# Performance work log

Hardware: AMD Instinct MI355X
Metric: run time of the kernel (lower is better)

Reference implementation:

```python
import jax, jax.numpy as jnp
import numpy as np

B, S, D = 8, 1024, 1152
H = 16
HD = D // H
HID = int(D * 4.0)
LN_EPS = 1e-5


def layer_norm(x, w, b):
    m = jnp.mean(x, axis=-1, keepdims=True)
    v = jnp.mean(jnp.square(x - m), axis=-1, keepdims=True)
    return (x - m) * jax.lax.rsqrt(v + LN_EPS) * w + b


def modulate(x, shift, scale):
    # shift/scale: [B, D] broadcast over seq
    return x * (1.0 + scale[:, None, :]) + shift[:, None, :]


def setup_inputs() -> dict:
    key = jax.random.key(0)
    ks = jax.random.split(key, 16)
    s = 0.02
    return {
        "x": jax.random.normal(ks[0], (B, S, D), jnp.float32),
        "c": jax.random.normal(ks[1], (B, D), jnp.float32),
        "ln1_w": jnp.ones((D,), jnp.float32),
        "ln1_b": jnp.zeros((D,), jnp.float32),
        "wq": jax.random.normal(ks[2], (D, D), jnp.float32) * s,
        "wk": jax.random.normal(ks[3], (D, D), jnp.float32) * s,
        "wv": jax.random.normal(ks[4], (D, D), jnp.float32) * s,
        "wo": jax.random.normal(ks[5], (D, D), jnp.float32) * s,
        "wo_b": jnp.zeros((D,), jnp.float32),
        "ln2_w": jnp.ones((D,), jnp.float32),
        "ln2_b": jnp.zeros((D,), jnp.float32),
        "fc1_w": jax.random.normal(ks[6], (D, HID), jnp.float32) * s,
        "fc1_b": jnp.zeros((HID,), jnp.float32),
        "fc2_w": jax.random.normal(ks[7], (HID, D), jnp.float32) * s,
        "fc2_b": jnp.zeros((D,), jnp.float32),
        "ada_w": jax.random.normal(ks[8], (D, 6 * D), jnp.float32) * s,
        "ada_b": jnp.zeros((6 * D,), jnp.float32),
    }


def attention(x, wq, wk, wv, wo, wo_b):
    b, s, d = x.shape
    q = (x @ wq).reshape(b, s, H, HD).transpose(0, 2, 1, 3)  # [B,H,S,hd]
    k = (x @ wk).reshape(b, s, H, HD).transpose(0, 2, 1, 3)
    v = (x @ wv).reshape(b, s, H, HD).transpose(0, 2, 1, 3)
    scale = 1.0 / np.sqrt(HD).astype(np.float32)
    att = jnp.einsum("bhqd,bhkd->bhqk", q, k) * scale
    att = jax.nn.softmax(att, axis=-1)
    out = jnp.einsum("bhqk,bhkd->bhqd", att, v)
    out = out.transpose(0, 2, 1, 3).reshape(b, s, d)
    return out @ wo + wo_b


def reference(x, c, ln1_w, ln1_b, wq, wk, wv, wo, wo_b, ln2_w, ln2_b,
              fc1_w, fc1_b, fc2_w, fc2_b, ada_w, ada_b):
    mod = jax.nn.silu(c) @ ada_w + ada_b  # [B, 6D]
    sh_msa, sc_msa, g_msa, sh_mlp, sc_mlp, g_mlp = jnp.split(mod, 6, axis=1)
    h = modulate(layer_norm(x, ln1_w, ln1_b), sh_msa, sc_msa)
    x = x + g_msa[:, None, :] * attention(h, wq, wk, wv, wo, wo_b)
    h = modulate(layer_norm(x, ln2_w, ln2_b), sh_mlp, sc_mlp)
    h = jax.nn.gelu(h @ fc1_w + fc1_b, approximate=False) @ fc2_w + fc2_b
    x = x + g_mlp[:, None, :] * h
    return x
```

## Files before the change

kernel.cpp:

```cpp
#include <hip/hip_runtime.h>
#include <hip/hip_bf16.h>


typedef unsigned short u16;
typedef unsigned int u32;
typedef __attribute__((ext_vector_type(8))) short bf16x8;
typedef __attribute__((ext_vector_type(4))) float f32x4;

#define MFMA16(a, b, c) __builtin_amdgcn_mfma_f32_16x16x32_bf16((a), (b), (c), 0, 0, 0)

__device__ __forceinline__ u16 f2bf(float f) {
  __hip_bfloat16 h = __float2bfloat16(f);
  return __builtin_bit_cast(u16, h);
}

__device__ __forceinline__ void gload16(const u16* g, u16* l) {
  __builtin_amdgcn_global_load_lds(
      (const __attribute__((address_space(1))) unsigned int*)(const void*)g,
      (__attribute__((address_space(3))) unsigned int*)(void*)l, 16, 0, 0);
}

__global__ void k_silu(const float* __restrict__ c, float* __restrict__ o, int n) {
  int i = blockIdx.x * 256 + threadIdx.x;
  if (i < n) { float v = c[i]; o[i] = v / (1.f + __expf(-v)); }
}

__global__ __launch_bounds__(256) void k_modproj1(const float* __restrict__ sc,
                                                  const float* __restrict__ aw,
                                                  float* __restrict__ partial) {
  __shared__ float lc[8][144];
  int kc = blockIdx.y;
  for (int i = threadIdx.x; i < 1152; i += 256) {
    int b = i / 144, k = i % 144;
    lc[b][k] = sc[b * 1152 + kc * 144 + k];
  }
  __syncthreads();
  int j = blockIdx.x * 256 + threadIdx.x;
  float acc[8] = {0, 0, 0, 0, 0, 0, 0, 0};
  for (int k = 0; k < 144; ++k) {
    float w = aw[(size_t)(kc * 144 + k) * 6912 + j];
    #pragma unroll
    for (int b = 0; b < 8; ++b) acc[b] += lc[b][k] * w;
  }
  #pragma unroll
  for (int b = 0; b < 8; ++b) partial[((size_t)kc * 8 + b) * 6912 + j] = acc[b];
}

__global__ __launch_bounds__(256) void k_modproj2(const float* __restrict__ partial,
                                                  const float* __restrict__ ab,
                                                  float* __restrict__ mo) {
  int j = blockIdx.x * 256 + threadIdx.x;
  float bias = ab[j];
  #pragma unroll
  for (int b = 0; b < 8; ++b) {
    float s = 0.f;
    #pragma unroll
    for (int kc = 0; kc < 8; ++kc) s += partial[((size_t)kc * 8 + b) * 6912 + j];
    mo[(size_t)b * 6912 + j] = s + bias;
  }
}

__global__ __launch_bounds__(256) void k_tcvt(const float* __restrict__ in, u16* __restrict__ out,
                                              int K, int N) {
  __shared__ float t[32][33];
  int tx = threadIdx.x & 31, ty = threadIdx.x >> 5;
  size_t bx = (size_t)blockIdx.x * 32, by = (size_t)blockIdx.y * 32;
  #pragma unroll
  for (int i = 0; i < 4; ++i) t[ty + 8 * i][tx] = in[(by + ty + 8 * i) * N + bx + tx];
  __syncthreads();
  #pragma unroll
  for (int i = 0; i < 4; ++i) out[(bx + ty + 8 * i) * K + by + tx] = f2bf(t[tx][ty + 8 * i]);
}

__global__ __launch_bounds__(256) void k_lnmod(const float* __restrict__ xin,
                                               const float* __restrict__ w,
                                               const float* __restrict__ bs,
                                               const float* __restrict__ mo,
                                               int sh_off, int sc_off, u16* __restrict__ o) {
  int row = blockIdx.x;
  int b = row >> 10;
  int tid = threadIdx.x;
  const float4* x4 = (const float4*)(xin + (size_t)row * 1152);
  float4 v0 = x4[tid];
  float4 v1 = make_float4(0.f, 0.f, 0.f, 0.f);
  if (tid < 32) v1 = x4[256 + tid];
  float s = v0.x + v0.y + v0.z + v0.w + v1.x + v1.y + v1.z + v1.w;
  float sq = v0.x * v0.x + v0.y * v0.y + v0.z * v0.z + v0.w * v0.w +
             v1.x * v1.x + v1.y * v1.y + v1.z * v1.z + v1.w * v1.w;
  #pragma unroll
  for (int d = 32; d > 0; d >>= 1) { s += __shfl_down(s, d); sq += __shfl_down(sq, d); }
  __shared__ float ps[4], pq[4];
  int wid = tid >> 6, lane = tid & 63;
  if (lane == 0) { ps[wid] = s; pq[wid] = sq; }
  __syncthreads();
  float S = ps[0] + ps[1] + ps[2] + ps[3];
  float SQ = pq[0] + pq[1] + pq[2] + pq[3];
  float mean = S * (1.f / 1152.f);
  float var = SQ * (1.f / 1152.f) - mean * mean;
  float rs = rsqrtf(var + 1e-5f);
  const float* shp = mo + (size_t)b * 6912 + sh_off;
  const float* scp = mo + (size_t)b * 6912 + sc_off;
  u16* orow = o + (size_t)row * 1152;
  {
    int col = 4 * tid;
    ushort4 u; float y;
    y = (v0.x - mean) * rs * w[col + 0] + bs[col + 0]; u.x = f2bf(y * (1.f + scp[col + 0]) + shp[col + 0]);
    y = (v0.y - mean) * rs * w[col + 1] + bs[col + 1]; u.y = f2bf(y * (1.f + scp[col + 1]) + shp[col + 1]);
    y = (v0.z - mean) * rs * w[col + 2] + bs[col + 2]; u.z = f2bf(y * (1.f + scp[col + 2]) + shp[col + 2]);
    y = (v0.w - mean) * rs * w[col + 3] + bs[col + 3]; u.w = f2bf(y * (1.f + scp[col + 3]) + shp[col + 3]);
    *(ushort4*)&orow[col] = u;
  }
  if (tid < 32) {
    int col = 1024 + 4 * tid;
    ushort4 u; float y;
    y = (v1.x - mean) * rs * w[col + 0] + bs[col + 0]; u.x = f2bf(y * (1.f + scp[col + 0]) + shp[col + 0]);
    y = (v1.y - mean) * rs * w[col + 1] + bs[col + 1]; u.y = f2bf(y * (1.f + scp[col + 1]) + shp[col + 1]);
    y = (v1.z - mean) * rs * w[col + 2] + bs[col + 2]; u.z = f2bf(y * (1.f + scp[col + 2]) + shp[col + 2]);
    y = (v1.w - mean) * rs * w[col + 3] + bs[col + 3]; u.w = f2bf(y * (1.f + scp[col + 3]) + shp[col + 3]);
    *(ushort4*)&orow[col] = u;
  }
}

template <int EPI>
__global__ __launch_bounds__(256) void k_gemm(const u16* __restrict__ A, const u16* __restrict__ Bt,
                                              int Kst, int klen, u16* __restrict__ Cb,
                                              float* __restrict__ Cf,
                                              const float* __restrict__ bias,
                                              const float* __restrict__ res,
                                              const float* __restrict__ mo, int goff,
                                              u16* __restrict__ vt) {
  const int tid = threadIdx.x;
  const int w = tid >> 6, lane = tid & 63;
  const int wr = w >> 1, wc = w & 1;
  const int lr = lane & 15, kg = lane >> 4;

  const int nwg = gridDim.x * gridDim.y;
  const int id = blockIdx.y * gridDim.x + blockIdx.x;
  const int swz = (id & 7) * (nwg >> 3) + (id >> 3);
  const int tM = (swz / gridDim.x) * 128, tN = (swz % gridDim.x) * 128;
  const int N = gridDim.x * 128;
  const int koff = blockIdx.z * klen;

  __shared__ u16 lA[2][128 * 32];
  __shared__ u16 lB[2][128 * 32];
  f32x4 acc[4][4];
  #pragma unroll
  for (int m = 0; m < 4; ++m)
    #pragma unroll
    for (int n = 0; n < 4; ++n) acc[m][n] = f32x4{0.f, 0.f, 0.f, 0.f};

  const int lrow = lane >> 2, lseg = lane & 3;
  const u16* gA = A + (size_t)(tM + w * 32 + lrow) * Kst + lseg * 8 + koff;
  const u16* gB = Bt + (size_t)(tN + w * 32 + lrow) * Kst + lseg * 8 + koff;
  const size_t rstep = (size_t)16 * Kst;
  const int wo0 = (w * 32) * 32, wo1 = (w * 32 + 16) * 32;
  const int aoff = (wr * 64 + lr) * 32 + kg * 8;
  const int boff = (wc * 64 + lr) * 32 + kg * 8;

#define STAGE(buf, ks)                        \
  do {                                        \
    gload16(gA + (ks), lA[buf] + wo0);        \
    gload16(gA + rstep + (ks), lA[buf] + wo1);\
    gload16(gB + (ks), lB[buf] + wo0);        \
    gload16(gB + rstep + (ks), lB[buf] + wo1);\
  } while (0)

#define COMPUTE(buf)                                                                  \
  do {                                                                                \
    bf16x8 af[4], bfr[4];                                                             \
    _Pragma("unroll")                                                                 \
    for (int m = 0; m < 4; ++m) af[m] = *(const bf16x8*)&lA[buf][aoff + m * 16 * 32]; \
    _Pragma("unroll")                                                                 \
    for (int n = 0; n < 4; ++n) bfr[n] = *(const bf16x8*)&lB[buf][boff + n * 16 * 32];\
    _Pragma("unroll")                                                                 \
    for (int m = 0; m < 4; ++m)                                                       \
      _Pragma("unroll")                                                               \
      for (int n = 0; n < 4; ++n) acc[m][n] = MFMA16(af[m], bfr[n], acc[m][n]);       \
  } while (0)

  const int nt = klen >> 5;
  STAGE(0, 0);
  __syncthreads();
  int t = 1;
  for (; t + 1 < nt; t += 2) {
    STAGE(1, t * 32);
    COMPUTE(0);
    __syncthreads();
    STAGE(0, t * 32 + 32);
    COMPUTE(1);
    __syncthreads();
  }
  STAGE(1, t * 32);
  COMPUTE(0);
  __syncthreads();
  COMPUTE(1);
#undef STAGE
#undef COMPUTE

  if (EPI == 3) {
    #pragma unroll
    for (int m = 0; m < 4; ++m)
      #pragma unroll
      for (int n = 0; n < 4; ++n) {
        int gcol = tN + wc * 64 + n * 16 + lr;
        int s0 = tM + wr * 64 + m * 16 + kg * 4;
        if (tN < 2304) {
          #pragma unroll
          for (int r = 0; r < 4; ++r) Cb[(size_t)(s0 + r) * N + gcol] = f2bf(acc[m][n][r]);
        } else {
          int qq = gcol - 2304;
          int hh = qq / 72;
          int d = qq - hh * 72;
          int bb = s0 >> 10, sl = s0 & 1023;
          ushort4 u;
          u.x = f2bf(acc[m][n][0]); u.y = f2bf(acc[m][n][1]);
          u.z = f2bf(acc[m][n][2]); u.w = f2bf(acc[m][n][3]);
          *(ushort4*)&vt[(((size_t)bb * 16 + hh) * 72 + d) * 1024 + sl] = u;
        }
      }
  } else if (EPI == 4) {
    float* Po = Cf + (size_t)blockIdx.z * ((size_t)gridDim.y * 128) * N;
    #pragma unroll
    for (int m = 0; m < 4; ++m)
      #pragma unroll
      for (int n = 0; n < 4; ++n)
        #pragma unroll
        for (int r = 0; r < 4; ++r) {
          int grow = tM + wr * 64 + m * 16 + kg * 4 + r;
          int gcol = tN + wc * 64 + n * 16 + lr;
          Po[(size_t)grow * N + gcol] = acc[m][n][r];
        }
  } else {
    #pragma unroll
    for (int m = 0; m < 4; ++m)
      #pragma unroll
      for (int n = 0; n < 4; ++n)
        #pragma unroll
        for (int r = 0; r < 4; ++r) {
          int grow = tM + wr * 64 + m * 16 + kg * 4 + r;
          int gcol = tN + wc * 64 + n * 16 + lr;
          size_t idx = (size_t)grow * N + gcol;
          float v = acc[m][n][r];
          if (EPI == 1) {
            float g = mo[(size_t)(grow >> 10) * 6912 + goff + gcol];
            Cf[idx] = res[idx] + g * (v + bias[gcol]);
          } else {
            float z = v + bias[gcol];
            float z2 = z * z;
            float u = z * __fmaf_rn(z2, -0.0713548162f, -1.5957691216f);
            float e = __expf(u);
            float gel = z * __builtin_amdgcn_rcpf(1.f + e);
            Cb[idx] = f2bf(gel);
          }
        }
  }
}

__global__ __launch_bounds__(256) void k_fc2red(const float* __restrict__ p,
                                                const float* __restrict__ x1,
                                                const float* __restrict__ bias,
                                                const float* __restrict__ mo,
                                                float* __restrict__ out) {
  size_t i = ((size_t)blockIdx.x * 256 + threadIdx.x) * 4;
  int row = (int)(i / 1152);
  int col = (int)(i - (size_t)row * 1152);
  int b = row >> 10;
  float4 a0 = *(const float4*)(p + i);
  float4 a1 = *(const float4*)(p + 9437184ull + i);
  float4 r = *(const float4*)(x1 + i);
  const float* gp = mo + (size_t)b * 6912 + 5760 + col;
  const float* bp = bias + col;
  float4 o;
  o.x = r.x + gp[0] * (a0.x + a1.x + bp[0]);
  o.y = r.y + gp[1] * (a0.y + a1.y + bp[1]);
  o.z = r.z + gp[2] * (a0.z + a1.z + bp[2]);
  o.w = r.w + gp[3] * (a0.w + a1.w + bp[3]);
  *(float4*)(out + i) = o;
}

__global__ __launch_bounds__(256) void k_attn(const u16* __restrict__ QKV, const u16* __restrict__ Vt,
                                              u16* __restrict__ O) {
  const int tid = threadIdx.x;
  const int w = tid >> 6, lane = tid & 63;
  const int lr = lane & 15, kg = lane >> 4;
  int bx = blockIdx.x;
  bx = (bx & 7) * 256 + (bx >> 3);
  const int qt = bx & 15, h = (bx >> 4) & 15, b = bx >> 8;

  __shared__ u16 lQ[64][104];
  __shared__ u16 lK[64][104];
  __shared__ u16 lVt[80][72];
  __shared__ u16 lPt[4][16][72];

  const size_t qkbase = (size_t)b * 1024 * 3456 + (size_t)h * 72;
  const u16* Qg = QKV + qkbase;
  const u16* Kg = QKV + qkbase + 1152;
  const u16* Vg = Vt + ((size_t)(b * 16 + h) * 72) * 1024;

  const uint4 z4 = make_uint4(0, 0, 0, 0);
  for (int L = tid; L < 192; L += 256) {
    int r = L / 3, s = L - (L / 3) * 3;
    *(uint4*)&lQ[r][72 + s * 8] = z4;
    *(uint4*)&lK[r][72 + s * 8] = z4;
  }
  for (int L = tid; L < 72; L += 256) {
    int r = L / 9, s = L - (L / 9) * 9;
    *(uint4*)&lVt[72 + r][s * 8] = z4;
  }
  {
    int L = tid; int r = L / 9, s = L - r * 9;
    *(uint4*)&lQ[r][s * 8] = *(const uint4*)(Qg + (size_t)(qt * 64 + r) * 3456 + s * 8);
    L = tid + 256; r = L / 9; s = L - r * 9;
    *(uint4*)&lQ[r][s * 8] = *(const uint4*)(Qg + (size_t)(qt * 64 + r) * 3456 + s * 8);
    if (tid < 64) {
      L = tid + 512; r = L / 9; s = L - r * 9;
      *(uint4*)&lQ[r][s * 8] = *(const uint4*)(Qg + (size_t)(qt * 64 + r) * 3456 + s * 8);
    }
  }
  __syncthreads();

  bf16x8 bq[3];
  #pragma unroll
  for (int ks = 0; ks < 3; ++ks) bq[ks] = *(const bf16x8*)&lQ[w * 16 + lr][ks * 32 + kg * 8];

  const float scale = 0.11785113019775793f;
  float mrun = -1e30f, lrun = 0.f;
  f32x4 oacc[5];
  #pragma unroll
  for (int nd = 0; nd < 5; ++nd) oacc[nd] = f32x4{0.f, 0.f, 0.f, 0.f};

  for (int kt = 0; kt < 16; ++kt) {
    __syncthreads();
    {
      int L = tid; int r = L / 9, s = L - (L / 9) * 9;
      *(uint4*)&lK[r][s * 8] = *(const uint4*)(Kg + (size_t)(kt * 64 + r) * 3456 + s * 8);
      int d = tid >> 3, sg = tid & 7;
      *(uint4*)&lVt[d][sg * 8] = *(const uint4*)(Vg + (size_t)d * 1024 + kt * 64 + sg * 8);
      L = tid + 256; r = L / 9; s = L - r * 9;
      *(uint4*)&lK[r][s * 8] = *(const uint4*)(Kg + (size_t)(kt * 64 + r) * 3456 + s * 8);
      d = (tid + 256) >> 3; sg = tid & 7;
      *(uint4*)&lVt[d][sg * 8] = *(const uint4*)(Vg + (size_t)d * 1024 + kt * 64 + sg * 8);
      if (tid < 64) {
        L = tid + 512; r = L / 9; s = L - r * 9;
        *(uint4*)&lK[r][s * 8] = *(const uint4*)(Kg + (size_t)(kt * 64 + r) * 3456 + s * 8);
        d = (tid + 512) >> 3;
        *(uint4*)&lVt[d][sg * 8] = *(const uint4*)(Vg + (size_t)d * 1024 + kt * 64 + sg * 8);
      }
    }
    __syncthreads();

    f32x4 sfr[4];
    __builtin_amdgcn_s_setprio(1);
    #pragma unroll
    for (int kb = 0; kb < 4; ++kb) {
      f32x4 sv = f32x4{0.f, 0.f, 0.f, 0.f};
      #pragma unroll
      for (int ks = 0; ks < 3; ++ks) {
        bf16x8 ak = *(const bf16x8*)&lK[kb * 16 + lr][ks * 32 + kg * 8];
        sv = MFMA16(ak, bq[ks], sv);
      }
      sfr[kb] = sv;
    }
    __builtin_amdgcn_s_setprio(0);

    float mx = sfr[0][0];
    #pragma unroll
    for (int kb = 0; kb < 4; ++kb)
      #pragma unroll
      for (int r = 0; r < 4; ++r) mx = fmaxf(mx, sfr[kb][r]);
    mx = fmaxf(mx, __shfl_xor(mx, 16));
    mx = fmaxf(mx, __shfl_xor(mx, 32));
    mx *= scale;
    float mn = fmaxf(mrun, mx);
    float al = __expf(mrun - mn);
    mrun = mn;
    float sum = 0.f;
    #pragma unroll
    for (int kb = 0; kb < 4; ++kb) {
      #pragma unroll
      for (int rp = 0; rp < 2; ++rp) {
        float p0 = __expf(__fmaf_rn(sfr[kb][2 * rp], scale, -mn));
        float p1 = __expf(__fmaf_rn(sfr[kb][2 * rp + 1], scale, -mn));
        sum += p0 + p1;
        u32 pk = (u32)f2bf(p0) | ((u32)f2bf(p1) << 16);
        *(u32*)&lPt[w][lr][kb * 16 + kg * 4 + rp * 2] = pk;
      }
    }
    sum += __shfl_xor(sum, 16);
    sum += __shfl_xor(sum, 32);
    lrun = lrun * al + sum;
    #pragma unroll
    for (int nd = 0; nd < 5; ++nd)
      #pragma unroll
      for (int r = 0; r < 4; ++r) oacc[nd][r] *= al;

    __builtin_amdgcn_s_setprio(1);
    #pragma unroll
    for (int s = 0; s < 2; ++s) {
      bf16x8 bp = *(const bf16x8*)&lPt[w][lr][s * 32 + kg * 8];
      #pragma unroll
      for (int nd = 0; nd < 5; ++nd) {
        bf16x8 av = *(const bf16x8*)&lVt[nd * 16 + lr][s * 32 + kg * 8];
        oacc[nd] = MFMA16(av, bp, oacc[nd]);
      }
    }
    __builtin_amdgcn_s_setprio(0);
  }

  float inv = 1.f / lrun;
  size_t orow = ((size_t)b * 1024 + qt * 64 + w * 16 + lr) * 1152 + h * 72;
  #pragma unroll
  for (int nd = 0; nd < 5; ++nd) {
    int d0 = nd * 16 + kg * 4;
    if (d0 < 72) {
      ushort4 u;
      u.x = f2bf(oacc[nd][0] * inv);
      u.y = f2bf(oacc[nd][1] * inv);
      u.z = f2bf(oacc[nd][2] * inv);
      u.w = f2bf(oacc[nd][3] * inv);
      *(ushort4*)&O[orow + d0] = u;
    }
  }
}

extern "C" void kernel_launch(void* const* d_in, const int* in_sizes, int n_in,
                              void* d_out, int out_size, void* d_ws, size_t ws_size,
                              hipStream_t stream) {
  const float* x     = (const float*)d_in[0];
  const float* c     = (const float*)d_in[1];
  const float* ln1_w = (const float*)d_in[2];
  const float* ln1_b = (const float*)d_in[3];
  const float* wq    = (const float*)d_in[4];
  const float* wk    = (const float*)d_in[5];
  const float* wv    = (const float*)d_in[6];
  const float* wo    = (const float*)d_in[7];
  const float* wo_b  = (const float*)d_in[8];
  const float* ln2_w = (const float*)d_in[9];
  const float* ln2_b = (const float*)d_in[10];
  const float* fc1_w = (const float*)d_in[11];
  const float* fc1_b = (const float*)d_in[12];
  const float* fc2_w = (const float*)d_in[13];
  const float* fc2_b = (const float*)d_in[14];
  const float* ada_w = (const float*)d_in[15];
  const float* ada_b = (const float*)d_in[16];
  float* out = (float*)d_out;

  char* base = (char*)d_ws;
  size_t off = 0;
  auto alloc = [&](size_t nbytes) -> void* {
    void* p = base + off;
    off += (nbytes + 255) & ~(size_t)255;
    return p;
  };
  const size_t MD = 8192ull * 1152;
  float* silu_c = (float*)alloc(9216 * 4);
  float* partial = (float*)alloc(64ull * 6912 * 4);
  float* modb   = (float*)alloc(55296 * 4);
  u16* qkvT = (u16*)alloc(3456ull * 1152 * 2);
  u16* woT  = (u16*)alloc(1152ull * 1152 * 2);
  u16* fc1T = (u16*)alloc(4608ull * 1152 * 2);
  u16* fc2T = (u16*)alloc(1152ull * 4608 * 2);
  u16* hbuf = (u16*)alloc(MD * 2);
  float* x1 = (float*)alloc(MD * 4);
  u16* vtb  = (u16*)alloc(128ull * 72 * 1024 * 2);
  float* fc2p = (float*)alloc(2ull * MD * 4);
  u16* big  = (u16*)alloc(8192ull * 4608 * 2);
  u16* qkv = big;
  u16* m1 = big;

  k_silu<<<36, 256, 0, stream>>>(c, silu_c, 9216);
  k_modproj1<<<dim3(27, 8), 256, 0, stream>>>(silu_c, ada_w, partial);
  k_modproj2<<<27, 256, 0, stream>>>(partial, ada_b, modb);
  k_tcvt<<<dim3(36, 36), 256, 0, stream>>>(wq, qkvT, 1152, 1152);
  k_tcvt<<<dim3(36, 36), 256, 0, stream>>>(wk, qkvT + 1152ull * 1152, 1152, 1152);
  k_tcvt<<<dim3(36, 36), 256, 0, stream>>>(wv, qkvT + 2304ull * 1152, 1152, 1152);
  k_tcvt<<<dim3(36, 36), 256, 0, stream>>>(wo, woT, 1152, 1152);
  k_tcvt<<<dim3(144, 36), 256, 0, stream>>>(fc1_w, fc1T, 1152, 4608);
  k_tcvt<<<dim3(36, 144), 256, 0, stream>>>(fc2_w, fc2T, 4608, 1152);

  k_lnmod<<<8192, 256, 0, stream>>>(x, ln1_w, ln1_b, modb, 0, 1152, hbuf);
  k_gemm<3><<<dim3(27, 64), 256, 0, stream>>>(hbuf, qkvT, 1152, 1152, qkv, nullptr, nullptr, nullptr, nullptr, 0, vtb);
  k_attn<<<2048, 256, 0, stream>>>(qkv, vtb, hbuf);
  k_gemm<1><<<dim3(9, 64), 256, 0, stream>>>(hbuf, woT, 1152, 1152, nullptr, x1, wo_b, x, modb, 2304, nullptr);
  k_lnmod<<<8192, 256, 0, stream>>>(x1, ln2_w, ln2_b, modb, 3456, 4608, hbuf);
  k_gemm<2><<<dim3(36, 64), 256, 0, stream>>>(hbuf, fc1T, 1152, 1152, m1, nullptr, fc1_b, nullptr, nullptr, 0, nullptr);
  k_gemm<4><<<dim3(9, 64, 2), 256, 0, stream>>>(m1, fc2T, 4608, 2304, nullptr, fc2p, nullptr, nullptr, nullptr, 0, nullptr);
  k_fc2red<<<9216, 256, 0, stream>>>(fc2p, x1, fc2_b, modb, out);
}
```

Measured before the change: 603.2 us.

## Switch GEMM to 32x32 MFMA with swizzled LDS, bf16 split-K partials, fuse SiLU

The GEMM core moves from 16x16x32 to 32x32x16 bf16 MFMA with 2x2 accumulator tiles per wave. The LDS layout gets an XOR swizzle on the 16-byte segment index to cut bank conflicts on fragment reads. The fc2 split-K partials are now stored as bf16 rather than fp32, halving that round-trip traffic at some accuracy cost. The separate SiLU kernel is folded into the modulation projection load, removing one launch.

```diff
diff --git a/kernel.cpp b/kernel.cpp
--- a/kernel.cpp
+++ b/kernel.cpp
@@ -6,12 +6,19 @@
 typedef unsigned int u32;
 typedef __attribute__((ext_vector_type(8))) short bf16x8;
 typedef __attribute__((ext_vector_type(4))) float f32x4;
+typedef __attribute__((ext_vector_type(16))) float f32x16;
 
 #define MFMA16(a, b, c) __builtin_amdgcn_mfma_f32_16x16x32_bf16((a), (b), (c), 0, 0, 0)
+#define MFMA32(a, b, c) __builtin_amdgcn_mfma_f32_32x32x16_bf16((a), (b), (c), 0, 0, 0)
 
 __device__ __forceinline__ u16 f2bf(float f) {
   __hip_bfloat16 h = __float2bfloat16(f);
   return __builtin_bit_cast(u16, h);
+}
+
+__device__ __forceinline__ float bf2f(u16 u) {
+  u32 v = ((u32)u) << 16;
+  return __builtin_bit_cast(float, v);
 }
 
 __device__ __forceinline__ void gload16(const u16* g, u16* l) {
@@ -20,19 +27,15 @@
       (__attribute__((address_space(3))) unsigned int*)(void*)l, 16, 0, 0);
 }
 
-__global__ void k_silu(const float* __restrict__ c, float* __restrict__ o, int n) {
-  int i = blockIdx.x * 256 + threadIdx.x;
-  if (i < n) { float v = c[i]; o[i] = v / (1.f + __expf(-v)); }
-}
-
-__global__ __launch_bounds__(256) void k_modproj1(const float* __restrict__ sc,
+__global__ __launch_bounds__(256) void k_modproj1(const float* __restrict__ cc,
                                                   const float* __restrict__ aw,
                                                   float* __restrict__ partial) {
   __shared__ float lc[8][144];
   int kc = blockIdx.y;
   for (int i = threadIdx.x; i < 1152; i += 256) {
     int b = i / 144, k = i % 144;
-    lc[b][k] = sc[b * 1152 + kc * 144 + k];
+    float v = cc[b * 1152 + kc * 144 + k];
+    lc[b][k] = v / (1.f + __expf(-v));
   }
   __syncthreads();
   int j = blockIdx.x * 256 + threadIdx.x;
@@ -132,7 +135,7 @@
   const int tid = threadIdx.x;
   const int w = tid >> 6, lane = tid & 63;
   const int wr = w >> 1, wc = w & 1;
-  const int lr = lane & 15, kg = lane >> 4;
+  const int l31 = lane & 31, hi = lane >> 5;
 
   const int nwg = gridDim.x * gridDim.y;
   const int id = blockIdx.y * gridDim.x + blockIdx.x;
@@ -143,19 +146,25 @@
 
   __shared__ u16 lA[2][128 * 32];
   __shared__ u16 lB[2][128 * 32];
-  f32x4 acc[4][4];
-  #pragma unroll
-  for (int m = 0; m < 4; ++m)
-    #pragma unroll
-    for (int n = 0; n < 4; ++n) acc[m][n] = f32x4{0.f, 0.f, 0.f, 0.f};
+  f32x16 acc[2][2];
+  #pragma unroll
+  for (int m = 0; m < 2; ++m)
+    #pragma unroll
+    for (int n = 0; n < 2; ++n)
+      #pragma unroll
+      for (int r = 0; r < 16; ++r) acc[m][n][r] = 0.f;
 
   const int lrow = lane >> 2, lseg = lane & 3;
-  const u16* gA = A + (size_t)(tM + w * 32 + lrow) * Kst + lseg * 8 + koff;
-  const u16* gB = Bt + (size_t)(tN + w * 32 + lrow) * Kst + lseg * 8 + koff;
+  const int fl = (lrow & 3) ^ ((lrow >> 2) & 3);
+  const u16* gA = A + (size_t)(tM + w * 32 + lrow) * Kst + (lseg ^ fl) * 8 + koff;
+  const u16* gB = Bt + (size_t)(tN + w * 32 + lrow) * Kst + (lseg ^ fl) * 8 + koff;
   const size_t rstep = (size_t)16 * Kst;
   const int wo0 = (w * 32) * 32, wo1 = (w * 32 + 16) * 32;
-  const int aoff = (wr * 64 + lr) * 32 + kg * 8;
-  const int boff = (wc * 64 + lr) * 32 + kg * 8;
+  const int fr = (l31 & 3) ^ ((l31 >> 2) & 3);
+  const int c0 = (hi ^ fr) * 8;
+  const int c1 = ((hi ^ fr) ^ 2) * 8;
+  const int arow = (wr * 64 + l31) * 32;
+  const int brow = (wc * 64 + l31) * 32;
 
 #define STAGE(buf, ks)                        \
   do {                                        \
@@ -165,17 +174,24 @@
     gload16(gB + rstep + (ks), lB[buf] + wo1);\
   } while (0)
 
-#define COMPUTE(buf)                                                                  \
-  do {                                                                                \
-    bf16x8 af[4], bfr[4];                                                             \
-    _Pragma("unroll")                                                                 \
-    for (int m = 0; m < 4; ++m) af[m] = *(const bf16x8*)&lA[buf][aoff + m * 16 * 32]; \
-    _Pragma("unroll")                                                                 \
-    for (int n = 0; n < 4; ++n) bfr[n] = *(const bf16x8*)&lB[buf][boff + n * 16 * 32];\
-    _Pragma("unroll")                                                                 \
-    for (int m = 0; m < 4; ++m)                                                       \
-      _Pragma("unroll")                                                               \
-      for (int n = 0; n < 4; ++n) acc[m][n] = MFMA16(af[m], bfr[n], acc[m][n]);       \
+#define COMPUTE(buf)                                                            \
+  do {                                                                          \
+    bf16x8 a00 = *(const bf16x8*)&lA[buf][arow + c0];                           \
+    bf16x8 a01 = *(const bf16x8*)&lA[buf][arow + c1];                           \
+    bf16x8 a10 = *(const bf16x8*)&lA[buf][arow + 1024 + c0];                    \
+    bf16x8 a11 = *(const bf16x8*)&lA[buf][arow + 1024 + c1];                    \
+    bf16x8 b00 = *(const bf16x8*)&lB[buf][brow + c0];                           \
+    bf16x8 b01 = *(const bf16x8*)&lB[buf][brow + c1];                           \
+    bf16x8 b10 = *(const bf16x8*)&lB[buf][brow + 1024 + c0];                    \
+    bf16x8 b11 = *(const bf16x8*)&lB[buf][brow + 1024 + c1];                    \
+    acc[0][0] = MFMA32(a00, b00, acc[0][0]);                                    \
+    acc[0][1] = MFMA32(a00, b10, acc[0][1]);                                    \
+    acc[1][0] = MFMA32(a10, b00, acc[1][0]);                                    \
+    acc[1][1] = MFMA32(a10, b10, acc[1][1]);                                    \
+    acc[0][0] = MFMA32(a01, b01, acc[0][0]);                                    \
+    acc[0][1] = MFMA32(a01, b11, acc[0][1]);                                    \
+    acc[1][0] = MFMA32(a11, b01, acc[1][0]);                                    \
+    acc[1][1] = MFMA32(a11, b11, acc[1][1]);                                    \
   } while (0)
 
   const int nt = klen >> 5;
@@ -197,66 +213,58 @@
 #undef STAGE
 #undef COMPUTE
 
-  if (EPI == 3) {
-    #pragma unroll
-    for (int m = 0; m < 4; ++m)
-      #pragma unroll
-      for (int n = 0; n < 4; ++n) {
-        int gcol = tN + wc * 64 + n * 16 + lr;
-        int s0 = tM + wr * 64 + m * 16 + kg * 4;
-        if (tN < 2304) {
+  #pragma unroll
+  for (int m = 0; m < 2; ++m)
+    #pragma unroll
+    for (int n = 0; n < 2; ++n) {
+      int gcol = tN + wc * 64 + n * 32 + l31;
+      #pragma unroll
+      for (int q = 0; q < 4; ++q) {
+        int grow0 = tM + wr * 64 + m * 32 + hi * 4 + q * 8;
+        if (EPI == 3) {
+          if (tN < 2304) {
+            #pragma unroll
+            for (int r = 0; r < 4; ++r)
+              Cb[(size_t)(grow0 + r) * N + gcol] = f2bf(acc[m][n][q * 4 + r]);
+          } else {
+            int qq = gcol - 2304;
+            int hh = qq / 72;
+            int d = qq - hh * 72;
+            int bb = grow0 >> 10, sl = grow0 & 1023;
+            ushort4 u;
+            u.x = f2bf(acc[m][n][q * 4 + 0]); u.y = f2bf(acc[m][n][q * 4 + 1]);
+            u.z = f2bf(acc[m][n][q * 4 + 2]); u.w = f2bf(acc[m][n][q * 4 + 3]);
+            *(ushort4*)&vt[(((size_t)bb * 16 + hh) * 72 + d) * 1024 + sl] = u;
+          }
+        } else if (EPI == 5) {
+          u16* Po = Cb + (size_t)blockIdx.z * ((size_t)gridDim.y * 128) * N;
           #pragma unroll
-          for (int r = 0; r < 4; ++r) Cb[(size_t)(s0 + r) * N + gcol] = f2bf(acc[m][n][r]);
+          for (int r = 0; r < 4; ++r)
+            Po[(size_t)(grow0 + r) * N + gcol] = f2bf(acc[m][n][q * 4 + r]);
+        } else if (EPI == 1) {
+          float g = mo[(size_t)(grow0 >> 10) * 6912 + goff + gcol];
+          float bi = bias[gcol];
+          #pragma unroll
+          for (int r = 0; r < 4; ++r) {
+            size_t idx = (size_t)(grow0 + r) * N + gcol;
+            Cf[idx] = res[idx] + g * (acc[m][n][q * 4 + r] + bi);
+          }
         } else {
-          int qq = gcol - 2304;
-          int hh = qq / 72;
-          int d = qq - hh * 72;
-          int bb = s0 >> 10, sl = s0 & 1023;
-          ushort4 u;
-          u.x = f2bf(acc[m][n][0]); u.y = f2bf(acc[m][n][1]);
-          u.z = f2bf(acc[m][n][2]); u.w = f2bf(acc[m][n][3]);
-          *(ushort4*)&vt[(((size_t)bb * 16 + hh) * 72 + d) * 1024 + sl] = u;
-        }
-      }
-  } else if (EPI == 4) {
-    float* Po = Cf + (size_t)blockIdx.z * ((size_t)gridDim.y * 128) * N;
-    #pragma unroll
-    for (int m = 0; m < 4; ++m)
-      #pragma unroll
-      for (int n = 0; n < 4; ++n)
-        #pragma unroll
-        for (int r = 0; r < 4; ++r) {
-          int grow = tM + wr * 64 + m * 16 + kg * 4 + r;
-          int gcol = tN + wc * 64 + n * 16 + lr;
-          Po[(size_t)grow * N + gcol] = acc[m][n][r];
-        }
-  } else {
-    #pragma unroll
-    for (int m = 0; m < 4; ++m)
-      #pragma unroll
-      for (int n = 0; n < 4; ++n)
-        #pragma unroll
-        for (int r = 0; r < 4; ++r) {
-          int grow = tM + wr * 64 + m * 16 + kg * 4 + r;
-          int gcol = tN + wc * 64 + n * 16 + lr;
-          size_t idx = (size_t)grow * N + gcol;
-          float v = acc[m][n][r];
-          if (EPI == 1) {
-            float g = mo[(size_t)(grow >> 10) * 6912 + goff + gcol];
-            Cf[idx] = res[idx] + g * (v + bias[gcol]);
-          } else {
-            float z = v + bias[gcol];
+          float bi = bias[gcol];
+          #pragma unroll
+          for (int r = 0; r < 4; ++r) {
+            float z = acc[m][n][q * 4 + r] + bi;
             float z2 = z * z;
             float u = z * __fmaf_rn(z2, -0.0713548162f, -1.5957691216f);
             float e = __expf(u);
-            float gel = z * __builtin_amdgcn_rcpf(1.f + e);
-            Cb[idx] = f2bf(gel);
+            Cb[(size_t)(grow0 + r) * N + gcol] = f2bf(z * __builtin_amdgcn_rcpf(1.f + e));
           }
         }
-  }
-}
-
-__global__ __launch_bounds__(256) void k_fc2red(const float* __restrict__ p,
+      }
+    }
+}
+
+__global__ __launch_bounds__(256) void k_fc2red(const u16* __restrict__ p,
                                                 const float* __restrict__ x1,
                                                 const float* __restrict__ bias,
                                                 const float* __restrict__ mo,
@@ -265,16 +273,16 @@
   int row = (int)(i / 1152);
   int col = (int)(i - (size_t)row * 1152);
   int b = row >> 10;
-  float4 a0 = *(const float4*)(p + i);
-  float4 a1 = *(const float4*)(p + 9437184ull + i);
+  ushort4 a0 = *(const ushort4*)(p + i);
+  ushort4 a1 = *(const ushort4*)(p + 9437184ull + i);
   float4 r = *(const float4*)(x1 + i);
   const float* gp = mo + (size_t)b * 6912 + 5760 + col;
   const float* bp = bias + col;
   float4 o;
-  o.x = r.x + gp[0] * (a0.x + a1.x + bp[0]);
-  o.y = r.y + gp[1] * (a0.y + a1.y + bp[1]);
-  o.z = r.z + gp[2] * (a0.z + a1.z + bp[2]);
-  o.w = r.w + gp[3] * (a0.w + a1.w + bp[3]);
+  o.x = r.x + gp[0] * (bf2f(a0.x) + bf2f(a1.x) + bp[0]);
+  o.y = r.y + gp[1] * (bf2f(a0.y) + bf2f(a1.y) + bp[1]);
+  o.z = r.z + gp[2] * (bf2f(a0.z) + bf2f(a1.z) + bp[2]);
+  o.w = r.w + gp[3] * (bf2f(a0.w) + bf2f(a1.w) + bp[3]);
   *(float4*)(out + i) = o;
 }
 
@@ -453,7 +461,6 @@
     return p;
   };
   const size_t MD = 8192ull * 1152;
-  float* silu_c = (float*)alloc(9216 * 4);
   float* partial = (float*)alloc(64ull * 6912 * 4);
   float* modb   = (float*)alloc(55296 * 4);
   u16* qkvT = (u16*)alloc(3456ull * 1152 * 2);
@@ -463,13 +470,12 @@
   u16* hbuf = (u16*)alloc(MD * 2);
   float* x1 = (float*)alloc(MD * 4);
   u16* vtb  = (u16*)alloc(128ull * 72 * 1024 * 2);
-  float* fc2p = (float*)alloc(2ull * MD * 4);
+  u16* fc2p = (u16*)alloc(2ull * MD * 2);
   u16* big  = (u16*)alloc(8192ull * 4608 * 2);
   u16* qkv = big;
   u16* m1 = big;
 
-  k_silu<<<36, 256, 0, stream>>>(c, silu_c, 9216);
-  k_modproj1<<<dim3(27, 8), 256, 0, stream>>>(silu_c, ada_w, partial);
+  k_modproj1<<<dim3(27, 8), 256, 0, stream>>>(c, ada_w, partial);
   k_modproj2<<<27, 256, 0, stream>>>(partial, ada_b, modb);
   k_tcvt<<<dim3(36, 36), 256, 0, stream>>>(wq, qkvT, 1152, 1152);
   k_tcvt<<<dim3(36, 36), 256, 0, stream>>>(wk, qkvT + 1152ull * 1152, 1152, 1152);
@@ -484,6 +490,6 @@
   k_gemm<1><<<dim3(9, 64), 256, 0, stream>>>(hbuf, woT, 1152, 1152, nullptr, x1, wo_b, x, modb, 2304, nullptr);
   k_lnmod<<<8192, 256, 0, stream>>>(x1, ln2_w, ln2_b, modb, 3456, 4608, hbuf);
   k_gemm<2><<<dim3(36, 64), 256, 0, stream>>>(hbuf, fc1T, 1152, 1152, m1, nullptr, fc1_b, nullptr, nullptr, 0, nullptr);
-  k_gemm<4><<<dim3(9, 64, 2), 256, 0, stream>>>(m1, fc2T, 4608, 2304, nullptr, fc2p, nullptr, nullptr, nullptr, 0, nullptr);
+  k_gemm<5><<<dim3(9, 64, 2), 256, 0, stream>>>(m1, fc2T, 4608, 2304, fc2p, nullptr, nullptr, nullptr, nullptr, 0, nullptr);
   k_fc2red<<<9216, 256, 0, stream>>>(fc2p, x1, fc2_b, modb, out);
 }
```

New measurement: 583.6 us. 1.03x faster.
